# Optimization experiments

Hardware: AMD Instinct MI355X
Metric: run time of the kernel (lower is better)

The kernel has to match this reference:

```python
import jax, jax.numpy as jnp
import numpy as np

N = 100000
E = 800000
IN_DIM = 256
H = 4
C = 32          # per-head hidden dim
SLOPE = 0.2


def gat_conv(x, W, att_src, att_dst, bias, src, dst):
    """PyG GATConv (single input tensor => lin_src applied to both src and dst),
    concat=True, add_self_loops=False, eval mode (no attn dropout).
    x: [N, F_in], W: [H*C, F_in], att_src/att_dst: [H, C], bias: [H*C].
    Returns [N, H*C]."""
    n = x.shape[0]
    xp = (x @ W.T).reshape(n, H, C)                    # [N,H,C]
    a_src = jnp.einsum('nhc,hc->nh', xp, att_src)      # [N,H]
    a_dst = jnp.einsum('nhc,hc->nh', xp, att_dst)      # [N,H]
    e = a_src[src] + a_dst[dst]                        # [E,H]
    e = jax.nn.leaky_relu(e, SLOPE)
    # segment softmax over incoming edges of each dst node
    m = jax.ops.segment_max(e, dst, num_segments=n)    # [N,H]
    ex = jnp.exp(e - m[dst])                           # [E,H]
    s = jax.ops.segment_sum(ex, dst, num_segments=n)   # [N,H]
    alpha = ex / (s[dst] + 1e-16)                      # [E,H]
    msg = xp[src] * alpha[:, :, None]                  # [E,H,C]
    out = jax.ops.segment_sum(msg, dst, num_segments=n)  # [N,H,C]
    return out.reshape(n, H * C) + bias


def setup_inputs() -> dict:
    key = jax.random.key(0)
    ks = jax.random.split(key, 12)
    x = jax.random.normal(ks[0], (N, IN_DIM), dtype=jnp.float32)
    edge_index = jax.random.randint(ks[1], (2, E), 0, N, dtype=jnp.int64)
    g = 1.414

    def xavier(k, shape):
        fan_in, fan_out = shape[-1], int(np.prod(shape[:-1]))
        std = g * np.sqrt(2.0 / (fan_in + fan_out))
        return jax.random.normal(k, shape, dtype=jnp.float32) * std

    W0 = xavier(ks[2], (H * C, IN_DIM))
    att_src0 = xavier(ks[3], (H, C))
    att_dst0 = xavier(ks[4], (H, C))
    b0 = jnp.zeros((H * C,), dtype=jnp.float32)
    W1 = xavier(ks[5], (H * C, H * C))
    att_src1 = xavier(ks[6], (H, C))
    att_dst1 = xavier(ks[7], (H, C))
    b1 = jnp.zeros((H * C,), dtype=jnp.float32)
    return {"x": x, "edge_index": edge_index,
            "W0": W0, "att_src0": att_src0, "att_dst0": att_dst0, "b0": b0,
            "W1": W1, "att_src1": att_src1, "att_dst1": att_dst1, "b1": b1}


def reference(x, edge_index, W0, att_src0, att_dst0, b0, W1, att_src1, att_dst1, b1):
    src, dst = edge_index[0], edge_index[1]
    h = gat_conv(x, W0, att_src0, att_dst0, b0, src, dst)
    h = jax.nn.relu(h)                 # activation on all but last layer
    h = gat_conv(h, W1, att_src1, att_dst1, b1, src, dst)
    # encoding=False => no last activation; head is Identity
    return h
```

## Files before the change

kernel.cpp:

```cpp
#include <hip/hip_runtime.h>
#include <hip/hip_bf16.h>
#include <cstdint>
#include <cstddef>
#include <type_traits>

#define SLOPE 0.2f

typedef __attribute__((ext_vector_type(8))) short short8v;
typedef __attribute__((ext_vector_type(4))) float float4v;

__device__ inline ushort f2bf(float f) {
  uint u = __float_as_uint(f);
  uint r = (u + 0x7FFFu + ((u >> 16) & 1u)) >> 16;
  return (ushort)r;
}
__device__ inline float bf2f(ushort u) {
  return __uint_as_float(((uint)u) << 16);
}
__device__ inline float bflo(uint u) { return __uint_as_float(u << 16); }
__device__ inline float bfhi(uint u) { return __uint_as_float(u & 0xffff0000u); }

__device__ inline short8v pack8(float4 a, float4 b) {
  uint4 r;
  r.x = (uint)f2bf(a.x) | ((uint)f2bf(a.y) << 16);
  r.y = (uint)f2bf(a.z) | ((uint)f2bf(a.w) << 16);
  r.z = (uint)f2bf(b.x) | ((uint)f2bf(b.y) << 16);
  r.w = (uint)f2bf(b.z) | ((uint)f2bf(b.w) << 16);
  return __builtin_bit_cast(short8v, r);
}
__device__ inline float lrelu(float v) { return (v > 0.f) ? v : SLOPE * v; }


__global__ void k_wconv(const float* __restrict__ W0, const float* __restrict__ W1,
                        ushort* __restrict__ Wb0, ushort* __restrict__ Wb1) {
  int i = blockIdx.x * 256 + threadIdx.x;
  if (i < 128 * 256) Wb0[i] = f2bf(W0[i]);
  if (i < 128 * 128) Wb1[i] = f2bf(W1[i]);
}


__global__ void k_count(const int* __restrict__ dst, int* __restrict__ counts, int E) {
  int e = blockIdx.x * 256 + threadIdx.x;
  if (e < E) atomicAdd(&counts[dst[e]], 1);
}

__global__ void k_scan1(const int* __restrict__ counts, int* __restrict__ excl,
                        int* __restrict__ bsums, int N) {
  __shared__ int lds[256];
  int tid = threadIdx.x;
  int base = blockIdx.x * 2048 + tid * 8;
  int v[8];
  int ts = 0;
#pragma unroll
  for (int i = 0; i < 8; i++) {
    int idx = base + i;
    int t = (idx < N) ? counts[idx] : 0;
    v[i] = ts;
    ts += t;
  }
  lds[tid] = ts;
  __syncthreads();
  for (int off = 1; off < 256; off <<= 1) {
    int t = (tid >= off) ? lds[tid - off] : 0;
    __syncthreads();
    lds[tid] += t;
    __syncthreads();
  }
  int texcl = (tid > 0) ? lds[tid - 1] : 0;
#pragma unroll
  for (int i = 0; i < 8; i++) {
    int idx = base + i;
    if (idx < N) excl[idx] = texcl + v[i];
  }
  if (tid == 255) bsums[blockIdx.x] = lds[255];
}

__global__ void k_scan2(int* bsums, int nb) {
  __shared__ int lds[256];
  int tid = threadIdx.x;
  int v = (tid < nb) ? bsums[tid] : 0;
  lds[tid] = v;
  __syncthreads();
  for (int off = 1; off < 256; off <<= 1) {
    int t = (tid >= off) ? lds[tid - off] : 0;
    __syncthreads();
    lds[tid] += t;
    __syncthreads();
  }
  if (tid < nb) bsums[tid] = (tid > 0) ? lds[tid - 1] : 0;
}

__global__ void k_scan3(int* __restrict__ excl, int* __restrict__ cursor,
                        const int* __restrict__ bsums, int N) {
  int tid = threadIdx.x;
  int off = bsums[blockIdx.x];
  int base = blockIdx.x * 2048 + tid * 8;
#pragma unroll
  for (int i = 0; i < 8; i++) {
    int idx = base + i;
    if (idx < N) {
      int val = excl[idx] + off;
      excl[idx] = val;
      cursor[idx] = val;
    }
  }
}

__global__ void k_fill(const int* __restrict__ src, const int* __restrict__ dst,
                       int* __restrict__ cursor, int* __restrict__ src_sorted, int E) {
  int e = blockIdx.x * 256 + threadIdx.x;
  if (e < E) {
    int d = dst[e];
    int pos = atomicAdd(&cursor[d], 1);
    src_sorted[pos] = src[e];
  }
}


template <typename AT, int K>
__global__ __launch_bounds__(256, 4) void k_gemm_lds(
    const AT* __restrict__ A, const ushort* __restrict__ Wb,
    const float* __restrict__ att_src, const float* __restrict__ att_dst,
    ushort* __restrict__ C, float* __restrict__ a_src, float* __restrict__ a_dst,
    int M) {
  constexpr int KH = 128;
  constexpr int LDW = KH + 8;
  __shared__ ushort Ws[128 * LDW];
  const int tid = threadIdx.x;
  const int wave = tid >> 6, lane = tid & 63;
  const int fr = lane & 15, fq = lane >> 4;
  const int bm = blockIdx.x * 64;
  const int r0 = bm + wave * 16 + fr;
  const int rc0 = min(r0, M - 1);
  const AT* arow = A + (size_t)rc0 * K + fq * 8;

  const int sr = tid >> 1;
  const int scb = (tid & 1) * (KH / 2);
  const ushort* wrow = Wb + (size_t)sr * K + scb;
  ushort* drow = &Ws[sr * LDW + scb];

#pragma unroll
  for (int i = 0; i < KH / 16; i++)
    *(uint4*)(drow + i * 8) = *(const uint4*)(wrow + i * 8);

  float4v acc[8] = {};

  if constexpr (std::is_same<AT, float>::value) {
    float4 a0[4][2];
#pragma unroll
    for (int s = 0; s < 4; s++) {
      const float* p = arow + s * 32;
      a0[s][0] = *(const float4*)p;
      a0[s][1] = *(const float4*)(p + 4);
    }
    __syncthreads();
#pragma unroll
    for (int s = 0; s < 4; s++) {
      short8v af = pack8(a0[s][0], a0[s][1]);
#pragma unroll
      for (int t = 0; t < 8; t++) {
        short8v bfr = *(const short8v*)&Ws[(t * 16 + fr) * LDW + s * 32 + fq * 8];
        acc[t] = __builtin_amdgcn_mfma_f32_16x16x32_bf16(af, bfr, acc[t], 0, 0, 0);
      }
    }
    float4 a1[4][2];
#pragma unroll
    for (int s = 0; s < 4; s++) {
      const float* p = arow + KH + s * 32;
      a1[s][0] = *(const float4*)p;
      a1[s][1] = *(const float4*)(p + 4);
    }
    __syncthreads();
#pragma unroll
    for (int i = 0; i < KH / 16; i++)
      *(uint4*)(drow + i * 8) = *(const uint4*)(wrow + KH + i * 8);
    __syncthreads();
#pragma unroll
    for (int s = 0; s < 4; s++) {
      short8v af = pack8(a1[s][0], a1[s][1]);
#pragma unroll
      for (int t = 0; t < 8; t++) {
        short8v bfr = *(const short8v*)&Ws[(t * 16 + fr) * LDW + s * 32 + fq * 8];
        acc[t] = __builtin_amdgcn_mfma_f32_16x16x32_bf16(af, bfr, acc[t], 0, 0, 0);
      }
    }
  } else {
    short8v a0[4];
#pragma unroll
    for (int s = 0; s < 4; s++)
      a0[s] = *(const short8v*)(arow + s * 32);
    __syncthreads();
#pragma unroll
    for (int s = 0; s < 4; s++) {
#pragma unroll
      for (int t = 0; t < 8; t++) {
        short8v bfr = *(const short8v*)&Ws[(t * 16 + fr) * LDW + s * 32 + fq * 8];
        acc[t] = __builtin_amdgcn_mfma_f32_16x16x32_bf16(a0[s], bfr, acc[t], 0, 0, 0);
      }
    }
  }

  float asc[8], adc[8];
#pragma unroll
  for (int t = 0; t < 8; t++) {
    asc[t] = att_src[t * 16 + fr];
    adc[t] = att_dst[t * 16 + fr];
  }

#pragma unroll
  for (int j = 0; j < 4; j++) {
    int row = bm + wave * 16 + fq * 4 + j;
    bool ok = row < M;
    if (ok) {
#pragma unroll
      for (int t = 0; t < 8; t++)
        C[(size_t)row * 128 + t * 16 + fr] = f2bf(acc[t][j]);
    }
    float ps[4], pd[4];
#pragma unroll
    for (int h = 0; h < 4; h++) {
      ps[h] = acc[2 * h][j] * asc[2 * h] + acc[2 * h + 1][j] * asc[2 * h + 1];
      pd[h] = acc[2 * h][j] * adc[2 * h] + acc[2 * h + 1][j] * adc[2 * h + 1];
    }
#pragma unroll
    for (int off = 1; off < 16; off <<= 1) {
#pragma unroll
      for (int h = 0; h < 4; h++) {
        ps[h] += __shfl_xor(ps[h], off);
        pd[h] += __shfl_xor(pd[h], off);
      }
    }
    if (ok && fr == 0) {
      *(float4*)&a_src[(size_t)row * 4] = make_float4(ps[0], ps[1], ps[2], ps[3]);
      *(float4*)&a_dst[(size_t)row * 4] = make_float4(pd[0], pd[1], pd[2], pd[3]);
    }
  }
}


__global__ __launch_bounds__(256) void k_msum(const int* __restrict__ ssort,
                                              const float* __restrict__ a_src,
                                              const float* __restrict__ a_dst,
                                              const int* __restrict__ indptr,
                                              const int* __restrict__ counts,
                                              float* __restrict__ m_buf,
                                              float* __restrict__ inv_buf, int N) {
  int n = blockIdx.x * 256 + threadIdx.x;
  if (n >= N) return;
  int deg = counts[n], start = indptr[n];
  const int* sp = ssort + start;
  float4 ad = *(const float4*)&a_dst[(size_t)n * 4];

  float4 ma = make_float4(-INFINITY, -INFINITY, -INFINITY, -INFINITY);
  float4 mb = ma;
  int i = 0;
  for (; i + 2 <= deg; i += 2) {
    int s0 = sp[i], s1 = sp[i + 1];
    float4 e0 = *(const float4*)&a_src[(size_t)s0 * 4];
    float4 e1 = *(const float4*)&a_src[(size_t)s1 * 4];
    ma.x = fmaxf(ma.x, lrelu(e0.x + ad.x)); ma.y = fmaxf(ma.y, lrelu(e0.y + ad.y));
    ma.z = fmaxf(ma.z, lrelu(e0.z + ad.z)); ma.w = fmaxf(ma.w, lrelu(e0.w + ad.w));
    mb.x = fmaxf(mb.x, lrelu(e1.x + ad.x)); mb.y = fmaxf(mb.y, lrelu(e1.y + ad.y));
    mb.z = fmaxf(mb.z, lrelu(e1.z + ad.z)); mb.w = fmaxf(mb.w, lrelu(e1.w + ad.w));
  }
  for (; i < deg; i++) {
    int s0 = sp[i];
    float4 e0 = *(const float4*)&a_src[(size_t)s0 * 4];
    ma.x = fmaxf(ma.x, lrelu(e0.x + ad.x)); ma.y = fmaxf(ma.y, lrelu(e0.y + ad.y));
    ma.z = fmaxf(ma.z, lrelu(e0.z + ad.z)); ma.w = fmaxf(ma.w, lrelu(e0.w + ad.w));
  }
  float4 m;
  m.x = fmaxf(ma.x, mb.x); m.y = fmaxf(ma.y, mb.y);
  m.z = fmaxf(ma.z, mb.z); m.w = fmaxf(ma.w, mb.w);

  float4 sa = make_float4(0.f, 0.f, 0.f, 0.f), sb = sa;
  i = 0;
  for (; i + 2 <= deg; i += 2) {
    int s0 = sp[i], s1 = sp[i + 1];
    float4 e0 = *(const float4*)&a_src[(size_t)s0 * 4];
    float4 e1 = *(const float4*)&a_src[(size_t)s1 * 4];
    sa.x += __expf(lrelu(e0.x + ad.x) - m.x); sa.y += __expf(lrelu(e0.y + ad.y) - m.y);
    sa.z += __expf(lrelu(e0.z + ad.z) - m.z); sa.w += __expf(lrelu(e0.w + ad.w) - m.w);
    sb.x += __expf(lrelu(e1.x + ad.x) - m.x); sb.y += __expf(lrelu(e1.y + ad.y) - m.y);
    sb.z += __expf(lrelu(e1.z + ad.z) - m.z); sb.w += __expf(lrelu(e1.w + ad.w) - m.w);
  }
  for (; i < deg; i++) {
    int s0 = sp[i];
    float4 e0 = *(const float4*)&a_src[(size_t)s0 * 4];
    sa.x += __expf(lrelu(e0.x + ad.x) - m.x); sa.y += __expf(lrelu(e0.y + ad.y) - m.y);
    sa.z += __expf(lrelu(e0.z + ad.z) - m.z); sa.w += __expf(lrelu(e0.w + ad.w) - m.w);
  }
  float4 inv;
  inv.x = 1.f / (sa.x + sb.x + 1e-16f); inv.y = 1.f / (sa.y + sb.y + 1e-16f);
  inv.z = 1.f / (sa.z + sb.z + 1e-16f); inv.w = 1.f / (sa.w + sb.w + 1e-16f);
  *(float4*)&m_buf[(size_t)n * 4] = m;
  *(float4*)&inv_buf[(size_t)n * 4] = inv;
}


template <bool RELU, typename OT>
__global__ __launch_bounds__(256) void k_agg(const ushort* __restrict__ xp,
                                             const float* __restrict__ a_src,
                                             const float* __restrict__ a_dst,
                                             const int* __restrict__ src_sorted,
                                             const int* __restrict__ indptr,
                                             const int* __restrict__ counts,
                                             const float* __restrict__ m_buf,
                                             const float* __restrict__ inv_buf,
                                             const float* __restrict__ bias,
                                             OT* __restrict__ out, int N) {
  int tid = threadIdx.x;
  int n = blockIdx.x * 8 + (tid >> 5);
  if (n >= N) return;
  int c4 = tid & 31;
  int h = c4 >> 3;
  int deg = counts[n];
  int start = indptr[n];
  const int* sp = src_sorted + start;
  const ushort* xpc = xp + c4 * 4;
  const float* asrc_h = a_src + h;
  float ad = a_dst[(size_t)n * 4 + h];
  float m = m_buf[(size_t)n * 4 + h];
  float inv = inv_buf[(size_t)n * 4 + h];

  float a0 = 0.f, a1 = 0.f, a2 = 0.f, a3 = 0.f;
  int i = 0;
  for (; i + 4 <= deg; i += 4) {
    int s0 = sp[i], s1 = sp[i + 1], s2 = sp[i + 2], s3 = sp[i + 3];
    float e0 = asrc_h[(size_t)s0 * 4], e1 = asrc_h[(size_t)s1 * 4];
    float e2 = asrc_h[(size_t)s2 * 4], e3 = asrc_h[(size_t)s3 * 4];
    uint2 v0 = *(const uint2*)(xpc + (size_t)s0 * 128);
    uint2 v1 = *(const uint2*)(xpc + (size_t)s1 * 128);
    uint2 v2 = *(const uint2*)(xpc + (size_t)s2 * 128);
    uint2 v3 = *(const uint2*)(xpc + (size_t)s3 * 128);
    float x0 = __expf(lrelu(e0 + ad) - m), x1 = __expf(lrelu(e1 + ad) - m);
    float x2 = __expf(lrelu(e2 + ad) - m), x3 = __expf(lrelu(e3 + ad) - m);
    a0 = fmaf(bflo(v0.x), x0, a0); a1 = fmaf(bfhi(v0.x), x0, a1);
    a2 = fmaf(bflo(v0.y), x0, a2); a3 = fmaf(bfhi(v0.y), x0, a3);
    a0 = fmaf(bflo(v1.x), x1, a0); a1 = fmaf(bfhi(v1.x), x1, a1);
    a2 = fmaf(bflo(v1.y), x1, a2); a3 = fmaf(bfhi(v1.y), x1, a3);
    a0 = fmaf(bflo(v2.x), x2, a0); a1 = fmaf(bfhi(v2.x), x2, a1);
    a2 = fmaf(bflo(v2.y), x2, a2); a3 = fmaf(bfhi(v2.y), x2, a3);
    a0 = fmaf(bflo(v3.x), x3, a0); a1 = fmaf(bfhi(v3.x), x3, a1);
    a2 = fmaf(bflo(v3.y), x3, a2); a3 = fmaf(bfhi(v3.y), x3, a3);
  }
  for (; i < deg; i++) {
    int s0 = sp[i];
    float x0 = __expf(lrelu(asrc_h[(size_t)s0 * 4] + ad) - m);
    uint2 v0 = *(const uint2*)(xpc + (size_t)s0 * 128);
    a0 = fmaf(bflo(v0.x), x0, a0); a1 = fmaf(bfhi(v0.x), x0, a1);
    a2 = fmaf(bflo(v0.y), x0, a2); a3 = fmaf(bfhi(v0.y), x0, a3);
  }

  float4 bv = *(const float4*)&bias[c4 * 4];
  float o0 = fmaf(a0, inv, bv.x);
  float o1 = fmaf(a1, inv, bv.y);
  float o2 = fmaf(a2, inv, bv.z);
  float o3 = fmaf(a3, inv, bv.w);
  if (RELU) {
    o0 = fmaxf(o0, 0.f); o1 = fmaxf(o1, 0.f);
    o2 = fmaxf(o2, 0.f); o3 = fmaxf(o3, 0.f);
  }
  if constexpr (std::is_same<OT, float>::value) {
    *(float4*)&out[(size_t)n * 128 + c4 * 4] = make_float4(o0, o1, o2, o3);
  } else {
    uint2 pk;
    pk.x = (uint)f2bf(o0) | ((uint)f2bf(o1) << 16);
    pk.y = (uint)f2bf(o2) | ((uint)f2bf(o3) << 16);
    *(uint2*)&((ushort*)out)[(size_t)n * 128 + c4 * 4] = pk;
  }
}


extern "C" void kernel_launch(void* const* d_in, const int* in_sizes, int n_in,
                              void* d_out, int out_size, void* d_ws, size_t ws_size,
                              hipStream_t stream) {
  const float* x   = (const float*)d_in[0];
  const int*   ei  = (const int*)d_in[1];
  const float* W0  = (const float*)d_in[2];
  const float* as0 = (const float*)d_in[3];
  const float* ad0 = (const float*)d_in[4];
  const float* b0  = (const float*)d_in[5];
  const float* W1  = (const float*)d_in[6];
  const float* as1 = (const float*)d_in[7];
  const float* ad1 = (const float*)d_in[8];
  const float* b1  = (const float*)d_in[9];

  const int N = in_sizes[0] / 256;
  const int E = in_sizes[1] / 2;
  const int* src = ei;
  const int* dst = ei + E;

  char* ws = (char*)d_ws;
  size_t off = 0;
  auto alloc = [&](size_t bytes) -> void* {
    void* p = ws + off;
    off += (bytes + 255) & ~(size_t)255;
    return p;
  };
  ushort* xp    = (ushort*)alloc((size_t)N * 128 * 2);
  ushort* hbuf  = (ushort*)alloc((size_t)N * 128 * 2);
  float* a_src  = (float*)alloc((size_t)N * 4 * 4);
  float* a_dst  = (float*)alloc((size_t)N * 4 * 4);
  float* m_buf  = (float*)alloc((size_t)N * 4 * 4);
  float* i_buf  = (float*)alloc((size_t)N * 4 * 4);
  int*   counts = (int*)alloc((size_t)N * 4);
  int*   indptr = (int*)alloc((size_t)N * 4);
  int*   cursor = (int*)alloc((size_t)N * 4);
  int*   ssort  = (int*)alloc((size_t)E * 4);
  int*   bsums  = (int*)alloc(256 * 4);
  ushort* Wb0   = (ushort*)alloc((size_t)128 * 256 * 2);
  ushort* Wb1   = (ushort*)alloc((size_t)128 * 128 * 2);

  hipMemsetAsync(counts, 0, (size_t)N * 4, stream);
  int eb = (E + 255) / 256;
  int nb = (N + 2047) / 2048;
  k_wconv<<<128, 256, 0, stream>>>(W0, W1, Wb0, Wb1);
  k_count<<<eb, 256, 0, stream>>>(dst, counts, E);
  k_scan1<<<nb, 256, 0, stream>>>(counts, indptr, bsums, N);
  k_scan2<<<1, 256, 0, stream>>>(bsums, nb);
  k_scan3<<<nb, 256, 0, stream>>>(indptr, cursor, bsums, N);
  k_fill<<<eb, 256, 0, stream>>>(src, dst, cursor, ssort, E);

  int gb = (N + 63) / 64;
  int nb256 = (N + 255) / 256;
  int gb8 = (N + 7) / 8;

  k_gemm_lds<float, 256><<<gb, 256, 0, stream>>>(x, Wb0, as0, ad0, xp,
                                                 a_src, a_dst, N);
  k_msum<<<nb256, 256, 0, stream>>>(ssort, a_src, a_dst, indptr, counts,
                                    m_buf, i_buf, N);
  k_agg<true, ushort><<<gb8, 256, 0, stream>>>(xp, a_src, a_dst, ssort, indptr,
                                               counts, m_buf, i_buf, b0, hbuf, N);

  k_gemm_lds<ushort, 128><<<gb, 256, 0, stream>>>(hbuf, Wb1, as1, ad1, xp,
                                                  a_src, a_dst, N);
  k_msum<<<nb256, 256, 0, stream>>>(ssort, a_src, a_dst, indptr, counts,
                                    m_buf, i_buf, N);
  k_agg<false, float><<<gb8, 256, 0, stream>>>(xp, a_src, a_dst, ssort, indptr,
                                               counts, m_buf, i_buf, b1,
                                               (float*)d_out, N);
}
```

Baseline: 286.8 us.

## Fuse segment max/sum softmax stats into aggregation kernel and drop memset

Removes the separate per-node max/sum kernel. Each aggregation wave now computes the softmax max and denominator itself: 8 lanes per head stride over the incoming edges and reduce with xor shuffles. This drops two launches and the m/inv buffer round trips through memory. The separate counts memset is also folded into the weight-conversion kernel as int4 zeroing. The cost is an extra pair of gathered a_src passes inside the aggregation kernel. The counts zeroing assumes N is a multiple of 4.

```diff
diff --git a/kernel.cpp b/kernel.cpp
--- a/kernel.cpp
+++ b/kernel.cpp
@@ -31,11 +31,13 @@
 __device__ inline float lrelu(float v) { return (v > 0.f) ? v : SLOPE * v; }
 
 
-__global__ void k_wconv(const float* __restrict__ W0, const float* __restrict__ W1,
-                        ushort* __restrict__ Wb0, ushort* __restrict__ Wb1) {
+__global__ void k_init(const float* __restrict__ W0, const float* __restrict__ W1,
+                       ushort* __restrict__ Wb0, ushort* __restrict__ Wb1,
+                       int4* __restrict__ counts4, int n4) {
   int i = blockIdx.x * 256 + threadIdx.x;
   if (i < 128 * 256) Wb0[i] = f2bf(W0[i]);
   if (i < 128 * 128) Wb1[i] = f2bf(W1[i]);
+  if (i < n4) counts4[i] = make_int4(0, 0, 0, 0);
 }
 
 
@@ -238,66 +240,6 @@
 }
 
 
-__global__ __launch_bounds__(256) void k_msum(const int* __restrict__ ssort,
-                                              const float* __restrict__ a_src,
-                                              const float* __restrict__ a_dst,
-                                              const int* __restrict__ indptr,
-                                              const int* __restrict__ counts,
-                                              float* __restrict__ m_buf,
-                                              float* __restrict__ inv_buf, int N) {
-  int n = blockIdx.x * 256 + threadIdx.x;
-  if (n >= N) return;
-  int deg = counts[n], start = indptr[n];
-  const int* sp = ssort + start;
-  float4 ad = *(const float4*)&a_dst[(size_t)n * 4];
-
-  float4 ma = make_float4(-INFINITY, -INFINITY, -INFINITY, -INFINITY);
-  float4 mb = ma;
-  int i = 0;
-  for (; i + 2 <= deg; i += 2) {
-    int s0 = sp[i], s1 = sp[i + 1];
-    float4 e0 = *(const float4*)&a_src[(size_t)s0 * 4];
-    float4 e1 = *(const float4*)&a_src[(size_t)s1 * 4];
-    ma.x = fmaxf(ma.x, lrelu(e0.x + ad.x)); ma.y = fmaxf(ma.y, lrelu(e0.y + ad.y));
-    ma.z = fmaxf(ma.z, lrelu(e0.z + ad.z)); ma.w = fmaxf(ma.w, lrelu(e0.w + ad.w));
-    mb.x = fmaxf(mb.x, lrelu(e1.x + ad.x)); mb.y = fmaxf(mb.y, lrelu(e1.y + ad.y));
-    mb.z = fmaxf(mb.z, lrelu(e1.z + ad.z)); mb.w = fmaxf(mb.w, lrelu(e1.w + ad.w));
-  }
-  for (; i < deg; i++) {
-    int s0 = sp[i];
-    float4 e0 = *(const float4*)&a_src[(size_t)s0 * 4];
-    ma.x = fmaxf(ma.x, lrelu(e0.x + ad.x)); ma.y = fmaxf(ma.y, lrelu(e0.y + ad.y));
-    ma.z = fmaxf(ma.z, lrelu(e0.z + ad.z)); ma.w = fmaxf(ma.w, lrelu(e0.w + ad.w));
-  }
-  float4 m;
-  m.x = fmaxf(ma.x, mb.x); m.y = fmaxf(ma.y, mb.y);
-  m.z = fmaxf(ma.z, mb.z); m.w = fmaxf(ma.w, mb.w);
-
-  float4 sa = make_float4(0.f, 0.f, 0.f, 0.f), sb = sa;
-  i = 0;
-  for (; i + 2 <= deg; i += 2) {
-    int s0 = sp[i], s1 = sp[i + 1];
-    float4 e0 = *(const float4*)&a_src[(size_t)s0 * 4];
-    float4 e1 = *(const float4*)&a_src[(size_t)s1 * 4];
-    sa.x += __expf(lrelu(e0.x + ad.x) - m.x); sa.y += __expf(lrelu(e0.y + ad.y) - m.y);
-    sa.z += __expf(lrelu(e0.z + ad.z) - m.z); sa.w += __expf(lrelu(e0.w + ad.w) - m.w);
-    sb.x += __expf(lrelu(e1.x + ad.x) - m.x); sb.y += __expf(lrelu(e1.y + ad.y) - m.y);
-    sb.z += __expf(lrelu(e1.z + ad.z) - m.z); sb.w += __expf(lrelu(e1.w + ad.w) - m.w);
-  }
-  for (; i < deg; i++) {
-    int s0 = sp[i];
-    float4 e0 = *(const float4*)&a_src[(size_t)s0 * 4];
-    sa.x += __expf(lrelu(e0.x + ad.x) - m.x); sa.y += __expf(lrelu(e0.y + ad.y) - m.y);
-    sa.z += __expf(lrelu(e0.z + ad.z) - m.z); sa.w += __expf(lrelu(e0.w + ad.w) - m.w);
-  }
-  float4 inv;
-  inv.x = 1.f / (sa.x + sb.x + 1e-16f); inv.y = 1.f / (sa.y + sb.y + 1e-16f);
-  inv.z = 1.f / (sa.z + sb.z + 1e-16f); inv.w = 1.f / (sa.w + sb.w + 1e-16f);
-  *(float4*)&m_buf[(size_t)n * 4] = m;
-  *(float4*)&inv_buf[(size_t)n * 4] = inv;
-}
-
-
 template <bool RELU, typename OT>
 __global__ __launch_bounds__(256) void k_agg(const ushort* __restrict__ xp,
                                              const float* __restrict__ a_src,
@@ -305,8 +247,6 @@
                                              const int* __restrict__ src_sorted,
                                              const int* __restrict__ indptr,
                                              const int* __restrict__ counts,
-                                             const float* __restrict__ m_buf,
-                                             const float* __restrict__ inv_buf,
                                              const float* __restrict__ bias,
                                              OT* __restrict__ out, int N) {
   int tid = threadIdx.x;
@@ -314,14 +254,29 @@
   if (n >= N) return;
   int c4 = tid & 31;
   int h = c4 >> 3;
+  int l8 = c4 & 7;
   int deg = counts[n];
   int start = indptr[n];
   const int* sp = src_sorted + start;
   const ushort* xpc = xp + c4 * 4;
   const float* asrc_h = a_src + h;
   float ad = a_dst[(size_t)n * 4 + h];
-  float m = m_buf[(size_t)n * 4 + h];
-  float inv = inv_buf[(size_t)n * 4 + h];
+
+  float mloc = -INFINITY;
+  for (int i = l8; i < deg; i += 8)
+    mloc = fmaxf(mloc, lrelu(asrc_h[(size_t)sp[i] * 4] + ad));
+  mloc = fmaxf(mloc, __shfl_xor(mloc, 1));
+  mloc = fmaxf(mloc, __shfl_xor(mloc, 2));
+  mloc = fmaxf(mloc, __shfl_xor(mloc, 4));
+  const float m = mloc;
+
+  float sloc = 0.f;
+  for (int i = l8; i < deg; i += 8)
+    sloc += __expf(lrelu(asrc_h[(size_t)sp[i] * 4] + ad) - m);
+  sloc += __shfl_xor(sloc, 1);
+  sloc += __shfl_xor(sloc, 2);
+  sloc += __shfl_xor(sloc, 4);
+  const float inv = 1.f / (sloc + 1e-16f);
 
   float a0 = 0.f, a1 = 0.f, a2 = 0.f, a3 = 0.f;
   int i = 0;
@@ -402,8 +357,6 @@
   ushort* hbuf  = (ushort*)alloc((size_t)N * 128 * 2);
   float* a_src  = (float*)alloc((size_t)N * 4 * 4);
   float* a_dst  = (float*)alloc((size_t)N * 4 * 4);
-  float* m_buf  = (float*)alloc((size_t)N * 4 * 4);
-  float* i_buf  = (float*)alloc((size_t)N * 4 * 4);
   int*   counts = (int*)alloc((size_t)N * 4);
   int*   indptr = (int*)alloc((size_t)N * 4);
   int*   cursor = (int*)alloc((size_t)N * 4);
@@ -412,10 +365,10 @@
   ushort* Wb0   = (ushort*)alloc((size_t)128 * 256 * 2);
   ushort* Wb1   = (ushort*)alloc((size_t)128 * 128 * 2);
 
-  hipMemsetAsync(counts, 0, (size_t)N * 4, stream);
+  int n4 = N / 4;
   int eb = (E + 255) / 256;
   int nb = (N + 2047) / 2048;
-  k_wconv<<<128, 256, 0, stream>>>(W0, W1, Wb0, Wb1);
+  k_init<<<128, 256, 0, stream>>>(W0, W1, Wb0, Wb1, (int4*)counts, n4);
   k_count<<<eb, 256, 0, stream>>>(dst, counts, E);
   k_scan1<<<nb, 256, 0, stream>>>(counts, indptr, bsums, N);
   k_scan2<<<1, 256, 0, stream>>>(bsums, nb);
@@ -423,21 +376,15 @@
   k_fill<<<eb, 256, 0, stream>>>(src, dst, cursor, ssort, E);
 
   int gb = (N + 63) / 64;
-  int nb256 = (N + 255) / 256;
   int gb8 = (N + 7) / 8;
 
   k_gemm_lds<float, 256><<<gb, 256, 0, stream>>>(x, Wb0, as0, ad0, xp,
                                                  a_src, a_dst, N);
-  k_msum<<<nb256, 256, 0, stream>>>(ssort, a_src, a_dst, indptr, counts,
-                                    m_buf, i_buf, N);
   k_agg<true, ushort><<<gb8, 256, 0, stream>>>(xp, a_src, a_dst, ssort, indptr,
-                                               counts, m_buf, i_buf, b0, hbuf, N);
+                                               counts, b0, hbuf, N);
 
   k_gemm_lds<ushort, 128><<<gb, 256, 0, stream>>>(hbuf, Wb1, as1, ad1, xp,
                                                   a_src, a_dst, N);
-  k_msum<<<nb256, 256, 0, stream>>>(ssort, a_src, a_dst, indptr, counts,
-                                    m_buf, i_buf, N);
   k_agg<false, float><<<gb8, 256, 0, stream>>>(xp, a_src, a_dst, ssort, indptr,
-                                               counts, m_buf, i_buf, b1,
-                                               (float*)d_out, N);
-}
+                                               counts, b1, (float*)d_out, N);
+}
```

Result: faster. 279.1 us (-2.7%).
